# Kernel optimization log

Measured on AMD Instinct MI355X. Metric: run time of the kernel, lower is better.

Reference implementation:

```python
import jax, jax.numpy as jnp
import numpy as np

E = 768       # embedding_dim
H = 12        # num_heads
ID = 768      # inter_dim
HD = ID // H  # head_dim = 64
DHX = HD // 2  # 32
DHY = HD - DHX  # 32
HP, WP = 16, 16
P = HP * WP
BASE = 10000.0
SCALE = HD ** -0.5


def rot_half(x):
    x1 = x[..., 0::2]
    x2 = x[..., 1::2]
    return jnp.stack([-x2, x1], axis=-1).reshape(x.shape)


def apply_rope(x, cos, sin):
    cos = jnp.repeat(cos, 2, axis=-1)
    sin = jnp.repeat(sin, 2, axis=-1)
    return x * cos + rot_half(x) * sin


def rope_cache(L, dim, base):
    inv_freq = 1.0 / base ** (jnp.arange(0, dim, 2, dtype=jnp.float32) / dim)
    t = jnp.arange(L, dtype=jnp.float32)
    freqs = t[:, None] * inv_freq[None, :]  # [L, dim//2]
    return jnp.cos(freqs), jnp.sin(freqs)


def _rope_tables():
    yy, xx = jnp.meshgrid(jnp.arange(HP), jnp.arange(WP), indexing='ij')
    py = yy.reshape(P)
    px = xx.reshape(P)
    cos_x, sin_x = rope_cache(WP, DHX, BASE)
    cos_y, sin_y = rope_cache(HP, DHY, BASE)
    # gather per-patch tables, shape (1,1,P,1,D/2)
    cx = cos_x[px].reshape(1, 1, P, 1, DHX // 2)
    sx = sin_x[px].reshape(1, 1, P, 1, DHX // 2)
    cy = cos_y[py].reshape(1, 1, P, 1, DHY // 2)
    sy = sin_y[py].reshape(1, 1, P, 1, DHY // 2)
    return cx, sx, cy, sy


def setup_inputs() -> dict:
    key = jax.random.key(0)
    ks = jax.random.split(key, 8)
    B, T = 8, 16
    x = jax.random.normal(ks[0], (B, T, P, E), dtype=jnp.float32)
    s = 0.02
    return {
        'x': x,
        'Wq': jax.random.normal(ks[1], (E, ID), dtype=jnp.float32) * s,
        'bq': jnp.zeros((ID,), dtype=jnp.float32),
        'Wk': jax.random.normal(ks[2], (E, ID), dtype=jnp.float32) * s,
        'bk': jnp.zeros((ID,), dtype=jnp.float32),
        'Wv': jax.random.normal(ks[3], (E, ID), dtype=jnp.float32) * s,
        'bv': jnp.zeros((ID,), dtype=jnp.float32),
        'Wo': jax.random.normal(ks[4], (ID, E), dtype=jnp.float32) * s,
    }


def reference(x, Wq, bq, Wk, bk, Wv, bv, Wo):
    B, T, Pn, _ = x.shape
    q = (x @ Wq + bq).reshape(B, T, Pn, H, HD)
    k = (x @ Wk + bk).reshape(B, T, Pn, H, HD)
    v = (x @ Wv + bv).reshape(B, T, Pn, H, HD)

    cx, sx, cy, sy = _rope_tables()
    qx, qy = q[..., :DHX], q[..., DHX:]
    kx, ky = k[..., :DHX], k[..., DHX:]
    q = jnp.concatenate([apply_rope(qx, cx, sx), apply_rope(qy, cy, sy)], axis=-1)
    k = jnp.concatenate([apply_rope(kx, cx, sx), apply_rope(ky, cy, sy)], axis=-1)

    scores = jnp.einsum('btihd,btjhd->bthij', q, k) * SCALE
    probs = jax.nn.softmax(scores, axis=-1)
    y = jnp.einsum('bthij,btjhd->btihd', probs, v).reshape(B, T, Pn, ID)
    return y @ Wo
```

## Files before the change

kernel.cpp:

```cpp
#include <hip/hip_runtime.h>
#include <hip/hip_bf16.h>
#include <cstdint>
#include <cstddef>

typedef __bf16 bf16;
typedef __bf16 bf16x8 __attribute__((ext_vector_type(8)));
typedef __bf16 bf16x4 __attribute__((ext_vector_type(4)));
typedef float  f32x4  __attribute__((ext_vector_type(4)));

#define MFMA_BF16(a,b,c) __builtin_amdgcn_mfma_f32_16x16x32_bf16((a),(b),(c),0,0,0)

#define BB 8
#define TT 16
#define PP 256
#define EE 768
#define HH 12
#define HDD 64
#define NQKV 2304
#define MROWS 32768

__device__ __forceinline__ void gld_lds16(const bf16* g, bf16* l) {
  __builtin_amdgcn_global_load_lds((const __attribute__((address_space(1))) void*)g,
                                   (__attribute__((address_space(3))) void*)l, 16, 0, 0);
}

__global__ __launch_bounds__(256) void k_cvt_x(const float* __restrict__ x,
                                               bf16* __restrict__ xb) {
  const int64_t i = (int64_t)blockIdx.x * 256 + threadIdx.x;
  const float4* src = (const float4*)x;
  float4 a = src[i * 2];
  float4 b = src[i * 2 + 1];
  bf16x8 o;
  o[0] = (bf16)a.x; o[1] = (bf16)a.y; o[2] = (bf16)a.z; o[3] = (bf16)a.w;
  o[4] = (bf16)b.x; o[5] = (bf16)b.y; o[6] = (bf16)b.z; o[7] = (bf16)b.w;
  *(bf16x8*)(xb + i * 8) = o;
}

__global__ __launch_bounds__(256) void k_wt(const float* __restrict__ Wq,
                                            const float* __restrict__ Wk,
                                            const float* __restrict__ Wv,
                                            const float* __restrict__ Wo,
                                            bf16* __restrict__ wt) {
  __shared__ float tile[32][33];
  const int n0 = blockIdx.x * 32;
  const int k0 = blockIdx.y * 32;
  const float* W;
  int nc;
  if (n0 < 768)        { W = Wq; nc = n0; }
  else if (n0 < 1536)  { W = Wk; nc = n0 - 768; }
  else if (n0 < 2304)  { W = Wv; nc = n0 - 1536; }
  else                 { W = Wo; nc = n0 - 2304; }
  const int tx = threadIdx.x & 31, ty = threadIdx.x >> 5;
  for (int r = ty; r < 32; r += 8)
    tile[r][tx] = W[(int64_t)(k0 + r) * 768 + nc + tx];
  __syncthreads();
  for (int r = ty; r < 32; r += 8)
    wt[(int64_t)(n0 + r) * 768 + k0 + tx] = (bf16)tile[tx][r];
}

__global__ __launch_bounds__(512, 2) void k_qkv(const bf16* __restrict__ xb,
                                                const bf16* __restrict__ wt,
                                                const float* __restrict__ bq,
                                                const float* __restrict__ bk,
                                                const float* __restrict__ bv,
                                                bf16* __restrict__ qb,
                                                bf16* __restrict__ kb,
                                                bf16* __restrict__ vt) {
  extern __shared__ char smem_raw[];
  bf16* smem = (bf16*)smem_raw;
  const int tid = threadIdx.x;
  const int w = tid >> 6, lane = tid & 63, quad = lane >> 4, l16 = lane & 15;
  const int wr = w >> 2, wc = w & 3;
  const int kap = l16 & 7;
  const int bid = blockIdx.x;
  const int xcd = bid & 7;
  const int loc = bid >> 3;
  const int m0  = (xcd * 16 + loc / 9) * 256;
  const int n0  = (loc % 9) * 256;
  const int srow = w * 8 + (lane >> 3);
  const int cgo  = ((lane & 7) ^ ((lane >> 3) & 7)) * 8;
  const bf16* Ag = xb + (int64_t)(m0 + srow) * 768 + cgo;
  const bf16* Bg = wt + (int64_t)(n0 + srow) * 768 + cgo;

  auto stage = [&](int kt, int p) {
    bf16* LA = smem + p * 32768 + w * 512;
    bf16* LB = LA + 16384;
    const bf16* GA = Ag + kt * 64;
    const bf16* GB = Bg + kt * 64;
#pragma unroll
    for (int rd = 0; rd < 4; ++rd) {
      gld_lds16(GA + rd * 49152, LA + rd * 4096);
      gld_lds16(GB + rd * 49152, LB + rd * 4096);
    }
  };

  f32x4 acc[8][4] = {};
  stage(0, 0);
  __syncthreads();
  for (int t = 0; t < 12; ++t) {
    if (t < 11) stage(t + 1, (t + 1) & 1);
    __builtin_amdgcn_sched_barrier(0);
    const bf16* A = smem + (t & 1) * 32768;
    const bf16* B = A + 16384;
    bf16x8 bfr[4][2];
#pragma unroll
    for (int ni = 0; ni < 4; ++ni)
#pragma unroll
      for (int kk = 0; kk < 2; ++kk)
        bfr[ni][kk] = *(const bf16x8*)&B[(wc * 64 + ni * 16 + l16) * 64 +
                                         (((kk * 4 + quad) ^ kap) * 8)];
#pragma unroll
    for (int mh = 0; mh < 2; ++mh) {
      bf16x8 afr[4][2];
#pragma unroll
      for (int mi = 0; mi < 4; ++mi)
#pragma unroll
        for (int kk = 0; kk < 2; ++kk)
          afr[mi][kk] = *(const bf16x8*)&A[(wr * 128 + mh * 64 + mi * 16 + l16) * 64 +
                                           (((kk * 4 + quad) ^ kap) * 8)];
      __builtin_amdgcn_s_setprio(1);
#pragma unroll
      for (int mi = 0; mi < 4; ++mi)
#pragma unroll
        for (int ni = 0; ni < 4; ++ni)
#pragma unroll
          for (int kk = 0; kk < 2; ++kk)
            acc[mh * 4 + mi][ni] = MFMA_BF16(afr[mi][kk], bfr[ni][kk], acc[mh * 4 + mi][ni]);
      __builtin_amdgcn_s_setprio(0);
    }
    __syncthreads();
  }
  const int sec = n0 / 768;
  const float* bias_p = (sec == 0) ? bq : (sec == 1) ? bk : bv;
  if (sec == 2) {
#pragma unroll
    for (int ni = 0; ni < 4; ++ni) {
      const int ng = (n0 % 768) + wc * 64 + ni * 16 + l16;
      const int h = ng >> 6, hd = ng & 63;
      const float bias = bias_p[ng];
#pragma unroll
      for (int mi = 0; mi < 8; ++mi) {
        const int rb = m0 + wr * 128 + mi * 16 + quad * 4;
        const int bt = rb >> 8, p = rb & 255;
        bf16x4 pk;
#pragma unroll
        for (int r = 0; r < 4; ++r) pk[r] = (bf16)(acc[mi][ni][r] + bias);
        *(bf16x4*)&vt[((int64_t)(bt * 12 + h) * 64 + hd) * 256 + p] = pk;
      }
    }
  } else {
    bf16* dst = (sec == 0) ? qb : kb;
    const float L2C = 0.83048202372184058696f;
#pragma unroll
    for (int ni = 0; ni < 4; ++ni) {
      const int ng = (n0 % 768) + wc * 64 + ni * 16 + l16;
      const int h = ng >> 6, hd = ng & 63;
      const float bias = bias_p[ng];
      const int j = (hd & 31) >> 1;
      const float invf = exp2f(-(float)j * L2C);
      const bool odd = (hd & 1);
      const bool isx = (hd < 32);
#pragma unroll
      for (int mi = 0; mi < 8; ++mi) {
        const int rb = m0 + wr * 128 + mi * 16 + quad * 4;
        const int bt = rb >> 8;
        const int pb = rb & 255;
#pragma unroll
        for (int r = 0; r < 4; ++r) {
          const int p = pb + r;
          float v = acc[mi][ni][r] + bias;
          float pv = __shfl_xor(v, 1, 64);
          const int pos = isx ? (p & 15) : (p >> 4);
          float sn, cs;
          __sincosf((float)pos * invf, &sn, &cs);
          float o = odd ? (v * cs + pv * sn) : (v * cs - pv * sn);
          dst[((int64_t)(bt * 12 + h) * 256 + p) * 64 + hd] = (bf16)o;
        }
      }
    }
  }
}

__global__ __launch_bounds__(256) void k_attn(bf16* qy,
                                              const bf16* __restrict__ kb,
                                              const bf16* __restrict__ vt) {
  __shared__ __align__(16) bf16 plds[4][16 * 264];
  const int tid = threadIdx.x;
  const int w = tid >> 6, lane = tid & 63, quad = lane >> 4, l16 = lane & 15;
  const int64_t base = (int64_t)blockIdx.x * 16384;
  bf16* Q = qy + base;
  const bf16* K = kb + base;
  const bf16* V = vt + base;
  bf16* pl = plds[w];
  for (int s = 0; s < 4; ++s) {
    const int r0 = w * 64 + s * 16;
    bf16x8 qf0 = *(const bf16x8*)&Q[(r0 + l16) * 64 + quad * 8];
    bf16x8 qf1 = *(const bf16x8*)&Q[(r0 + l16) * 64 + 32 + quad * 8];
    f32x4 sacc[16] = {};
#pragma unroll
    for (int ct = 0; ct < 16; ++ct) {
      bf16x8 kf0 = *(const bf16x8*)&K[(ct * 16 + l16) * 64 + quad * 8];
      bf16x8 kf1 = *(const bf16x8*)&K[(ct * 16 + l16) * 64 + 32 + quad * 8];
      sacc[ct] = MFMA_BF16(qf0, kf0, sacc[ct]);
      sacc[ct] = MFMA_BF16(qf1, kf1, sacc[ct]);
    }
    float mx[4] = {-3e38f, -3e38f, -3e38f, -3e38f};
#pragma unroll
    for (int ct = 0; ct < 16; ++ct)
#pragma unroll
      for (int r = 0; r < 4; ++r) mx[r] = fmaxf(mx[r], sacc[ct][r]);
#pragma unroll
    for (int d = 1; d < 16; d <<= 1)
#pragma unroll
      for (int r = 0; r < 4; ++r) mx[r] = fmaxf(mx[r], __shfl_xor(mx[r], d, 64));
    float sm[4] = {0.f, 0.f, 0.f, 0.f};
#pragma unroll
    for (int ct = 0; ct < 16; ++ct)
#pragma unroll
      for (int r = 0; r < 4; ++r) {
        float e = __expf((sacc[ct][r] - mx[r]) * 0.125f);
        sacc[ct][r] = e;
        sm[r] += e;
      }
#pragma unroll
    for (int d = 1; d < 16; d <<= 1)
#pragma unroll
      for (int r = 0; r < 4; ++r) sm[r] += __shfl_xor(sm[r], d, 64);
#pragma unroll
    for (int ct = 0; ct < 16; ++ct)
#pragma unroll
      for (int r = 0; r < 4; ++r)
        pl[(quad * 4 + r) * 264 + ct * 16 + l16] = (bf16)sacc[ct][r];
    __syncthreads();
    f32x4 oacc[4] = {};
#pragma unroll
    for (int kc = 0; kc < 8; ++kc) {
      bf16x8 pf = *(const bf16x8*)&pl[l16 * 264 + kc * 32 + quad * 8];
#pragma unroll
      for (int nt = 0; nt < 4; ++nt) {
        bf16x8 vf = *(const bf16x8*)&V[(nt * 16 + l16) * 256 + kc * 32 + quad * 8];
        oacc[nt] = MFMA_BF16(pf, vf, oacc[nt]);
      }
    }
    float inv[4];
#pragma unroll
    for (int r = 0; r < 4; ++r) inv[r] = 1.0f / sm[r];
#pragma unroll
    for (int nt = 0; nt < 4; ++nt)
#pragma unroll
      for (int r = 0; r < 4; ++r)
        Q[(r0 + quad * 4 + r) * 64 + nt * 16 + l16] = (bf16)(oacc[nt][r] * inv[r]);
    __syncthreads();
  }
}

__global__ __launch_bounds__(256) void k_out(const bf16* __restrict__ yb,
                                             const bf16* __restrict__ wt,
                                             float* __restrict__ out) {
  __shared__ __align__(16) bf16 As[128 * 32];
  __shared__ __align__(16) bf16 Bs[128 * 32];
  const int tid = threadIdx.x;
  const int w = tid >> 6, lane = tid & 63, quad = lane >> 4, l16 = lane & 15;
  const int bid = blockIdx.x;
  const int xcd = bid & 7;
  const int loc = bid >> 3;
  const int m0  = (xcd * 32 + loc / 6) * 128;
  const int n0  = (loc % 6) * 128;
  const int bt = m0 >> 8, p0 = m0 & 255;
  const int arow = tid >> 2, aseg = (tid & 3) * 8;
  const bf16* Bg = wt + (int64_t)(2304 + n0 + arow) * 768 + aseg;
  bf16* AsW0 = As + (size_t)w * 512;
  bf16* AsW1 = As + 2048 + (size_t)w * 512;
  bf16* BsW0 = Bs + (size_t)w * 512;
  bf16* BsW1 = Bs + 2048 + (size_t)w * 512;
  const int mb = (w & 1) * 64, nb = (w >> 1) * 64;
  f32x4 acc[4][4] = {};
  for (int kt = 0; kt < 24; ++kt) {
    const int h = kt >> 1, hd0 = (kt & 1) * 32;
    const bf16* Ag = yb + ((int64_t)(bt * 12 + h) * 256 + p0 + arow) * 64 + hd0 + aseg;
    gld_lds16(Ag, AsW0);
    gld_lds16(Ag + 64 * 64, AsW1);
    gld_lds16(Bg + kt * 32, BsW0);
    gld_lds16(Bg + 64 * 768 + kt * 32, BsW1);
    __syncthreads();
    bf16x8 af[4], bfr[4];
#pragma unroll
    for (int i = 0; i < 4; ++i)
      af[i] = *(const bf16x8*)&As[(mb + i * 16 + l16) * 32 + quad * 8];
#pragma unroll
    for (int i = 0; i < 4; ++i)
      bfr[i] = *(const bf16x8*)&Bs[(nb + i * 16 + l16) * 32 + quad * 8];
#pragma unroll
    for (int mi = 0; mi < 4; ++mi)
#pragma unroll
      for (int ni = 0; ni < 4; ++ni)
        acc[mi][ni] = MFMA_BF16(af[mi], bfr[ni], acc[mi][ni]);
    __syncthreads();
  }
#pragma unroll
  for (int mi = 0; mi < 4; ++mi)
#pragma unroll
    for (int ni = 0; ni < 4; ++ni) {
      const int rg = m0 + mb + mi * 16 + quad * 4;
      const int cg = n0 + nb + ni * 16 + l16;
#pragma unroll
      for (int r = 0; r < 4; ++r)
        out[(int64_t)(rg + r) * 768 + cg] = acc[mi][ni][r];
    }
}

extern "C" void kernel_launch(void* const* d_in, const int* in_sizes, int n_in,
                              void* d_out, int out_size, void* d_ws, size_t ws_size,
                              hipStream_t stream) {
  const float* x  = (const float*)d_in[0];
  const float* Wq = (const float*)d_in[1];
  const float* bq = (const float*)d_in[2];
  const float* Wk = (const float*)d_in[3];
  const float* bk = (const float*)d_in[4];
  const float* Wv = (const float*)d_in[5];
  const float* bv = (const float*)d_in[6];
  const float* Wo = (const float*)d_in[7];
  float* out = (float*)d_out;

  uint8_t* ws = (uint8_t*)d_ws;
  const size_t SZ = (size_t)25165824 * 2;
  bf16* qy = (bf16*)ws;
  bf16* kb = (bf16*)(ws + SZ);
  bf16* vt = (bf16*)(ws + 2 * SZ);
  bf16* wt = (bf16*)(ws + 3 * SZ);
  bf16* xb = (bf16*)d_out;

  static int attr_set = 0;
  if (!attr_set) {
    (void)hipFuncSetAttribute((const void*)k_qkv,
                              hipFuncAttributeMaxDynamicSharedMemorySize, 131072);
    attr_set = 1;
  }

  k_cvt_x<<<12288, 256, 0, stream>>>(x, xb);
  k_wt<<<dim3(96, 24), 256, 0, stream>>>(Wq, Wk, Wv, Wo, wt);
  k_qkv<<<1152, 512, 131072, stream>>>(xb, wt, bq, bk, bv, qy, kb, vt);
  k_attn<<<1536, 256, 0, stream>>>(qy, kb, vt);
  k_out<<<1536, 256, 0, stream>>>(qy, wt, out);
}
```

Before: 526.5 us.

## Deepen QKV GEMM pipeline to 4 stages and enlarge output-projection tiles

The QKV GEMM moves from a 2-buffer, 64-wide K step to a 4-buffer ring of 32-wide K steps. Three stages are kept in flight and gated by explicit vmcnt waits plus a single barrier per iteration, so global-load latency is hidden behind more compute. The output projection is rewritten to use 512-thread blocks with 256x128 tiles, 64-wide K steps, double-buffered dynamic LDS with an XOR swizzle, and fewer blocks, which raises data reuse and overlaps loads with MFMA. Risks include hand-tuned waitcnt counts, a changed swizzle and lower occupancy in the output kernel.

```diff
diff --git a/kernel.cpp b/kernel.cpp
--- a/kernel.cpp
+++ b/kernel.cpp
@@ -71,64 +71,55 @@
   const int tid = threadIdx.x;
   const int w = tid >> 6, lane = tid & 63, quad = lane >> 4, l16 = lane & 15;
   const int wr = w >> 2, wc = w & 3;
-  const int kap = l16 & 7;
   const int bid = blockIdx.x;
   const int xcd = bid & 7;
   const int loc = bid >> 3;
   const int m0  = (xcd * 16 + loc / 9) * 256;
   const int n0  = (loc % 9) * 256;
-  const int srow = w * 8 + (lane >> 3);
-  const int cgo  = ((lane & 7) ^ ((lane >> 3) & 7)) * 8;
-  const bf16* Ag = xb + (int64_t)(m0 + srow) * 768 + cgo;
-  const bf16* Bg = wt + (int64_t)(n0 + srow) * 768 + cgo;
-
-  auto stage = [&](int kt, int p) {
-    bf16* LA = smem + p * 32768 + w * 512;
-    bf16* LB = LA + 16384;
-    const bf16* GA = Ag + kt * 64;
-    const bf16* GB = Bg + kt * 64;
-#pragma unroll
-    for (int rd = 0; rd < 4; ++rd) {
-      gld_lds16(GA + rd * 49152, LA + rd * 4096);
-      gld_lds16(GB + rd * 49152, LB + rd * 4096);
-    }
+  const int cg8 = (((lane & 3) ^ ((lane >> 3) & 3)) * 8);
+  const bf16* Ag0 = xb + (int64_t)(m0 + w * 16 + (lane >> 2)) * 768 + cg8;
+  const bf16* Bg0 = wt + (int64_t)(n0 + w * 16 + (lane >> 2)) * 768 + cg8;
+
+  auto stage = [&](int kt, int b) {
+    bf16* LA = smem + b * 16384 + w * 512;
+    bf16* LB = LA + 8192;
+    const bf16* GA = Ag0 + kt * 32;
+    const bf16* GB = Bg0 + kt * 32;
+    gld_lds16(GA, LA);
+    gld_lds16(GA + 128 * 768, LA + 4096);
+    gld_lds16(GB, LB);
+    gld_lds16(GB + 128 * 768, LB + 4096);
   };
 
   f32x4 acc[8][4] = {};
   stage(0, 0);
-  __syncthreads();
-  for (int t = 0; t < 12; ++t) {
-    if (t < 11) stage(t + 1, (t + 1) & 1);
+  stage(1, 1);
+  stage(2, 2);
+  const int rkey8 = ((l16 >> 1) & 3) * 8;
+  for (int t = 0; t < 24; ++t) {
+    if (t < 22)       { asm volatile("s_waitcnt vmcnt(8)" ::: "memory"); }
+    else if (t == 22) { asm volatile("s_waitcnt vmcnt(4)" ::: "memory"); }
+    else              { asm volatile("s_waitcnt vmcnt(0)" ::: "memory"); }
+    __builtin_amdgcn_s_barrier();
     __builtin_amdgcn_sched_barrier(0);
-    const bf16* A = smem + (t & 1) * 32768;
-    const bf16* B = A + 16384;
-    bf16x8 bfr[4][2];
+    if (t < 21) stage(t + 3, (t + 3) & 3);
+    const bf16* A = smem + (t & 3) * 16384;
+    const bf16* B = A + 8192;
+    bf16x8 bfr[4];
 #pragma unroll
     for (int ni = 0; ni < 4; ++ni)
-#pragma unroll
-      for (int kk = 0; kk < 2; ++kk)
-        bfr[ni][kk] = *(const bf16x8*)&B[(wc * 64 + ni * 16 + l16) * 64 +
-                                         (((kk * 4 + quad) ^ kap) * 8)];
-#pragma unroll
-    for (int mh = 0; mh < 2; ++mh) {
-      bf16x8 afr[4][2];
-#pragma unroll
-      for (int mi = 0; mi < 4; ++mi)
-#pragma unroll
-        for (int kk = 0; kk < 2; ++kk)
-          afr[mi][kk] = *(const bf16x8*)&A[(wr * 128 + mh * 64 + mi * 16 + l16) * 64 +
-                                           (((kk * 4 + quad) ^ kap) * 8)];
-      __builtin_amdgcn_s_setprio(1);
-#pragma unroll
-      for (int mi = 0; mi < 4; ++mi)
-#pragma unroll
-        for (int ni = 0; ni < 4; ++ni)
-#pragma unroll
-          for (int kk = 0; kk < 2; ++kk)
-            acc[mh * 4 + mi][ni] = MFMA_BF16(afr[mi][kk], bfr[ni][kk], acc[mh * 4 + mi][ni]);
-      __builtin_amdgcn_s_setprio(0);
-    }
-    __syncthreads();
+      bfr[ni] = *(const bf16x8*)&B[(wc * 64 + ni * 16 + l16) * 32 + ((quad * 8) ^ rkey8)];
+    bf16x8 afr[8];
+#pragma unroll
+    for (int mi = 0; mi < 8; ++mi)
+      afr[mi] = *(const bf16x8*)&A[(wr * 128 + mi * 16 + l16) * 32 + ((quad * 8) ^ rkey8)];
+    __builtin_amdgcn_s_setprio(1);
+#pragma unroll
+    for (int mi = 0; mi < 8; ++mi)
+#pragma unroll
+      for (int ni = 0; ni < 4; ++ni)
+        acc[mi][ni] = MFMA_BF16(afr[mi], bfr[ni], acc[mi][ni]);
+    __builtin_amdgcn_s_setprio(0);
   }
   const int sec = n0 / 768;
   const float* bias_p = (sec == 0) ? bq : (sec == 1) ? bk : bv;
@@ -254,55 +245,77 @@
   }
 }
 
-__global__ __launch_bounds__(256) void k_out(const bf16* __restrict__ yb,
-                                             const bf16* __restrict__ wt,
-                                             float* __restrict__ out) {
-  __shared__ __align__(16) bf16 As[128 * 32];
-  __shared__ __align__(16) bf16 Bs[128 * 32];
+__global__ __launch_bounds__(512, 2) void k_out(const bf16* __restrict__ yb,
+                                                const bf16* __restrict__ wt,
+                                                float* __restrict__ out) {
+  extern __shared__ char smem_raw[];
+  bf16* smem = (bf16*)smem_raw;
   const int tid = threadIdx.x;
   const int w = tid >> 6, lane = tid & 63, quad = lane >> 4, l16 = lane & 15;
+  const int wr = w >> 1, wc = w & 1;
   const int bid = blockIdx.x;
   const int xcd = bid & 7;
   const int loc = bid >> 3;
-  const int m0  = (xcd * 32 + loc / 6) * 128;
+  const int m0  = (xcd * 16 + loc / 6) * 256;
   const int n0  = (loc % 6) * 128;
-  const int bt = m0 >> 8, p0 = m0 & 255;
-  const int arow = tid >> 2, aseg = (tid & 3) * 8;
-  const bf16* Bg = wt + (int64_t)(2304 + n0 + arow) * 768 + aseg;
-  bf16* AsW0 = As + (size_t)w * 512;
-  bf16* AsW1 = As + 2048 + (size_t)w * 512;
-  bf16* BsW0 = Bs + (size_t)w * 512;
-  bf16* BsW1 = Bs + 2048 + (size_t)w * 512;
-  const int mb = (w & 1) * 64, nb = (w >> 1) * 64;
+  const int bt  = m0 >> 8;
+  const int srow = w * 8 + (lane >> 3);
+  const int cgo  = (((lane & 7) ^ ((lane >> 3) & 7)) * 8);
+  const bf16* Bg0 = wt + (int64_t)(2304 + n0 + srow) * 768 + cgo;
+
+  auto stage = [&](int kt, int p) {
+    bf16* LA = smem + p * 24576 + w * 512;
+    bf16* LB = smem + p * 24576 + 16384 + w * 512;
+    const bf16* GA = yb + (int64_t)(bt * 12 + kt) * 16384 + srow * 64 + cgo;
+    const bf16* GB = Bg0 + kt * 64;
+#pragma unroll
+    for (int rd = 0; rd < 4; ++rd)
+      gld_lds16(GA + rd * 4096, LA + rd * 4096);
+#pragma unroll
+    for (int rd = 0; rd < 2; ++rd)
+      gld_lds16(GB + rd * 49152, LB + rd * 4096);
+  };
+
   f32x4 acc[4][4] = {};
-  for (int kt = 0; kt < 24; ++kt) {
-    const int h = kt >> 1, hd0 = (kt & 1) * 32;
-    const bf16* Ag = yb + ((int64_t)(bt * 12 + h) * 256 + p0 + arow) * 64 + hd0 + aseg;
-    gld_lds16(Ag, AsW0);
-    gld_lds16(Ag + 64 * 64, AsW1);
-    gld_lds16(Bg + kt * 32, BsW0);
-    gld_lds16(Bg + 64 * 768 + kt * 32, BsW1);
+  stage(0, 0);
+  __syncthreads();
+  const int rkey8 = (l16 & 7) * 8;
+  for (int t = 0; t < 12; ++t) {
+    if (t < 11) stage(t + 1, (t + 1) & 1);
+    __builtin_amdgcn_sched_barrier(0);
+    const bf16* A = smem + (t & 1) * 24576;
+    const bf16* B = A + 16384;
+    bf16x8 bfr[4][2];
+#pragma unroll
+    for (int ni = 0; ni < 4; ++ni)
+#pragma unroll
+      for (int kk = 0; kk < 2; ++kk)
+        bfr[ni][kk] = *(const bf16x8*)&B[(wc * 64 + ni * 16 + l16) * 64 +
+                                         (((kk * 4 + quad) * 8) ^ rkey8)];
+    bf16x8 afr[4][2];
+#pragma unroll
+    for (int mi = 0; mi < 4; ++mi)
+#pragma unroll
+      for (int kk = 0; kk < 2; ++kk)
+        afr[mi][kk] = *(const bf16x8*)&A[(wr * 64 + mi * 16 + l16) * 64 +
+                                         (((kk * 4 + quad) * 8) ^ rkey8)];
+    __builtin_amdgcn_s_setprio(1);
+#pragma unroll
+    for (int mi = 0; mi < 4; ++mi)
+#pragma unroll
+      for (int ni = 0; ni < 4; ++ni)
+#pragma unroll
+        for (int kk = 0; kk < 2; ++kk)
+          acc[mi][ni] = MFMA_BF16(afr[mi][kk], bfr[ni][kk], acc[mi][ni]);
+    __builtin_amdgcn_s_setprio(0);
     __syncthreads();
-    bf16x8 af[4], bfr[4];
-#pragma unroll
-    for (int i = 0; i < 4; ++i)
-      af[i] = *(const bf16x8*)&As[(mb + i * 16 + l16) * 32 + quad * 8];
-#pragma unroll
-    for (int i = 0; i < 4; ++i)
-      bfr[i] = *(const bf16x8*)&Bs[(nb + i * 16 + l16) * 32 + quad * 8];
-#pragma unroll
-    for (int mi = 0; mi < 4; ++mi)
-#pragma unroll
-      for (int ni = 0; ni < 4; ++ni)
-        acc[mi][ni] = MFMA_BF16(af[mi], bfr[ni], acc[mi][ni]);
-    __syncthreads();
   }
 #pragma unroll
   for (int mi = 0; mi < 4; ++mi)
 #pragma unroll
     for (int ni = 0; ni < 4; ++ni) {
-      const int rg = m0 + mb + mi * 16 + quad * 4;
-      const int cg = n0 + nb + ni * 16 + l16;
+      const int rg = m0 + wr * 64 + mi * 16 + quad * 4;
+      const int cg = n0 + wc * 64 + ni * 16 + l16;
 #pragma unroll
       for (int r = 0; r < 4; ++r)
         out[(int64_t)(rg + r) * 768 + cg] = acc[mi][ni][r];
@@ -334,6 +347,8 @@
   if (!attr_set) {
     (void)hipFuncSetAttribute((const void*)k_qkv,
                               hipFuncAttributeMaxDynamicSharedMemorySize, 131072);
+    (void)hipFuncSetAttribute((const void*)k_out,
+                              hipFuncAttributeMaxDynamicSharedMemorySize, 98304);
     attr_set = 1;
   }
 
@@ -341,5 +356,5 @@
   k_wt<<<dim3(96, 24), 256, 0, stream>>>(Wq, Wk, Wv, Wo, wt);
   k_qkv<<<1152, 512, 131072, stream>>>(xb, wt, bq, bk, bv, qy, kb, vt);
   k_attn<<<1536, 256, 0, stream>>>(qy, kb, vt);
-  k_out<<<1536, 256, 0, stream>>>(qy, wt, out);
-}
+  k_out<<<768, 512, 98304, stream>>>(qy, wt, out);
+}
```

New measurement: 537.0 us. No clear change (+2.0%).
